# Performance work log

Measured on AMD Instinct MI355X. Metric: run time of the kernel, lower is better.

## Reference

```python
import jax, jax.numpy as jnp
import numpy as np

T, K, H, I, E = 8192, 2, 1024, 2816, 8


def setup_inputs() -> dict:
    key = jax.random.key(0)
    k1, k2, k3, k4, k5 = jax.random.split(key, 5)
    hidden_states = jax.random.normal(k1, (T, H), dtype=jnp.float32)
    expert_routing_table = jax.random.randint(k2, (T, K), 0, E)
    router_weights = jax.random.uniform(k3, (T, K), dtype=jnp.float32)
    # permuted_weights=True: weights stored so forward is x @ w
    # w13: fused gate+up proj [E, H, 2I]; w2: down proj [E, I, H]
    w13 = jax.random.normal(k4, (E, H, 2 * I), dtype=jnp.float32) * (1.0 / np.sqrt(H))
    w2 = jax.random.normal(k5, (E, I, H), dtype=jnp.float32) * (1.0 / np.sqrt(I))
    return {
        "hidden_states": hidden_states,
        "expert_routing_table": expert_routing_table,
        "router_weights": router_weights,
        "w13": w13,
        "w2": w2,
    }


def reference(hidden_states, expert_routing_table, router_weights, w13, w2):
    # Semantics of hpu.mixture_of_experts with activation='silu':
    # out[t] = sum_k rw[t,k] * ( (silu(x@w1g[e]) * (x@w1u[e])) @ w2[e] ), e = table[t,k]
    n_experts = w13.shape[0]
    inter = w2.shape[1]
    # per-token combine coefficient for each expert: [T, E]
    onehot = jax.nn.one_hot(expert_routing_table, n_experts, dtype=hidden_states.dtype)  # [T,K,E]
    coeff = jnp.einsum("tke,tk->te", onehot, router_weights)
    out = jnp.zeros_like(hidden_states)
    for e in range(n_experts):
        gu = hidden_states @ w13[e]            # [T, 2I]
        gate, up = gu[:, :inter], gu[:, inter:]
        h = jax.nn.silu(gate) * up             # [T, I]
        out = out + coeff[:, e:e + 1] * (h @ w2[e])
    return out
```

## Files before the change

### kernel.cpp

```cpp
#include <hip/hip_runtime.h>

typedef unsigned short u16;
typedef unsigned int u32;
typedef __bf16 bf16x8 __attribute__((ext_vector_type(8)));
typedef float f32x4 __attribute__((ext_vector_type(4)));
typedef u16 u16x4 __attribute__((ext_vector_type(4)));
typedef u16 u16x8 __attribute__((ext_vector_type(8)));

#define T_TOK 8192
#define HDIM 1024
#define IDIM 2816
#define NEXP 8
#define NPAIR (T_TOK * 2)
#define MAXRB 71

#define XB_OFF   (147456u)
#define W13T_OFF (XB_OFF + 16777216u)
#define W2T_OFF  (W13T_OFF + 92274688u)
#define H_OFF    (W2T_OFF + 46137344u)
#define WS_NEED  ((size_t)H_OFF + 102367232u)

__device__ __forceinline__ u16 f2bf(float f) {
  u32 u = __builtin_bit_cast(u32, f);
  u32 r = u + 0x7fffu + ((u >> 16) & 1u);
  return (u16)(r >> 16);
}

#define GLD16(g, l) __builtin_amdgcn_global_load_lds( \
    (const __attribute__((address_space(1))) void*)(g), \
    (__attribute__((address_space(3))) void*)(l), 16, 0, 0)

#define WAITVM(N) asm volatile("s_waitcnt vmcnt(" #N ")" ::: "memory")

__device__ __forceinline__ void pbar() {
  __builtin_amdgcn_sched_barrier(0);
  asm volatile("" ::: "memory");
  __builtin_amdgcn_s_barrier();
  asm volatile("" ::: "memory");
  __builtin_amdgcn_sched_barrier(0);
}

__global__ void init_meta(int* meta) {
  if (threadIdx.x < 16) meta[threadIdx.x] = 0;
}

__global__ void count_k(const int* __restrict__ routing, int* __restrict__ meta) {
  int i = blockIdx.x * 256 + threadIdx.x;
  if (i < NPAIR) atomicAdd(&meta[routing[i]], 1);
}

__global__ void scan_k(int* __restrict__ meta) {
  if (threadIdx.x == 0) {
    int rb = 0;
    for (int e = 0; e < NEXP; ++e) {
      meta[16 + e] = rb * 256;
      int nrb = (meta[e] + 255) >> 8;
      for (int i = 0; i < nrb; ++i) meta[32 + rb + i] = e;
      rb += nrb;
    }
    meta[24] = rb;
  }
}

__global__ void fill_pairs(int* __restrict__ pairs) {
  pairs[blockIdx.x * 256 + threadIdx.x] = -1;
}

__global__ void scatter_k(const int* __restrict__ routing, int* __restrict__ meta,
                          int* __restrict__ pairs, int* __restrict__ inv) {
  int i = blockIdx.x * 256 + threadIdx.x;
  if (i < NPAIR) {
    int e = routing[i];
    int pos = atomicAdd(&meta[8 + e], 1);
    int row = meta[16 + e] + pos;
    pairs[row] = i;
    inv[i] = row;
  }
}

__global__ void conv_x(const float* __restrict__ in, u16* __restrict__ out) {
  int i = blockIdx.x * 256 + threadIdx.x;
  float4 a = ((const float4*)in)[2 * i];
  float4 b = ((const float4*)in)[2 * i + 1];
  u16x8 o = { f2bf(a.x), f2bf(a.y), f2bf(a.z), f2bf(a.w),
              f2bf(b.x), f2bf(b.y), f2bf(b.z), f2bf(b.w) };
  ((u16x8*)out)[i] = o;
}

__global__ void transpose_cvt(const float* __restrict__ in, u16* __restrict__ out,
                              int R, int C) {
  __shared__ float tile[64][68];
  size_t base = (size_t)blockIdx.z * (size_t)R * (size_t)C;
  in += base; out += base;
  int t = threadIdx.x;
  int r0 = blockIdx.y * 64, c0 = blockIdx.x * 64;
  int lr = t >> 4, lc4 = (t & 15) * 4;
#pragma unroll
  for (int p = 0; p < 4; ++p) {
    float4 v = *(const float4*)&in[(size_t)(r0 + p * 16 + lr) * C + c0 + lc4];
    tile[p * 16 + lr][lc4] = v.x; tile[p * 16 + lr][lc4 + 1] = v.y;
    tile[p * 16 + lr][lc4 + 2] = v.z; tile[p * 16 + lr][lc4 + 3] = v.w;
  }
  __syncthreads();
  int oc = t >> 2, g0 = (t & 3) * 2;
#pragma unroll
  for (int gg = 0; gg < 2; ++gg) {
    int g = g0 + gg;
    u16x8 o = { f2bf(tile[g * 8 + 0][oc]), f2bf(tile[g * 8 + 1][oc]),
                f2bf(tile[g * 8 + 2][oc]), f2bf(tile[g * 8 + 3][oc]),
                f2bf(tile[g * 8 + 4][oc]), f2bf(tile[g * 8 + 5][oc]),
                f2bf(tile[g * 8 + 6][oc]), f2bf(tile[g * 8 + 7][oc]) };
    *(u16x8*)&out[(size_t)(c0 + oc) * R + r0 + g * 8] = o;
  }
}

__global__ __launch_bounds__(512, 2) void gemm1_k(
    const u16* __restrict__ Xb, const u16* __restrict__ W13T,
    const int* __restrict__ pairs, const int* __restrict__ meta,
    const float* __restrict__ rwf, u16* __restrict__ Hb) {
  int lin = blockIdx.x + 22 * blockIdx.y;
  int xcd = lin & 7, slot = lin >> 3;
  int flat = (xcd < 2) ? xcd * 196 + slot : 392 + (xcd - 2) * 195 + slot;
  int bx = flat / 71, rb = flat % 71;
  if (rb >= meta[24]) return;
  const int e = meta[32 + rb];
  const int bn0 = bx * 128;
  const int tid = threadIdx.x, lane = tid & 63, w = tid >> 6;
  const int wr = w >> 1, wc = w & 1;
  const int rowBase = rb * 256;

  __shared__ __align__(16) u16 lds[65536];
  char* const lb = (char*)lds;

  const int sr = tid >> 3;
  const int swk = ((tid & 7) << 4) ^ ((sr & 7) << 4);
  const u16* aS[4];
#pragma unroll
  for (int h = 0; h < 2; ++h)
#pragma unroll
    for (int j = 0; j < 2; ++j) {
      int pr = pairs[rowBase + h * 128 + j * 64 + sr];
      int tok = pr < 0 ? 0 : (pr >> 1);
      aS[h * 2 + j] = Xb + (size_t)tok * HDIM + (swk >> 1);
    }
  const u16* wBase = W13T + (size_t)e * (2 * IDIM) * HDIM;
  const u16* gS[2]; const u16* uS[2];
#pragma unroll
  for (int j = 0; j < 2; ++j) {
    int r = j * 64 + sr;
    gS[j] = wBase + (size_t)(bn0 + r) * HDIM + (swk >> 1);
    uS[j] = wBase + (size_t)(IDIM + bn0 + r) * HDIM + (swk >> 1);
  }

#define STG_A(b, h, kt) { GLD16(aS[(h)*2+0] + (kt)*64, lb + (b)*32768 + (h)*16384 + tid*16); \
                          GLD16(aS[(h)*2+1] + (kt)*64, lb + (b)*32768 + (h)*16384 + 8192 + tid*16); }
#define STG_G(b, kt)    { GLD16(gS[0] + (kt)*64, lb + 65536 + (b)*16384 + tid*16); \
                          GLD16(gS[1] + (kt)*64, lb + 65536 + (b)*16384 + 8192 + tid*16); }
#define STG_U(b, kt)    { GLD16(uS[0] + (kt)*64, lb + 98304 + (b)*16384 + tid*16); \
                          GLD16(uS[1] + (kt)*64, lb + 98304 + (b)*16384 + 8192 + tid*16); }

  const int l15 = lane & 15, l4 = lane >> 4, l7 = lane & 7;
  const int ko0 = (l4 * 16) ^ (l7 << 4);
  const int ko1 = (64 + l4 * 16) ^ (l7 << 4);
  const int aFB = (wr >> 1) * 16384 + ((wr & 1) * 64 + l15) * 128;
  const int bFB = (wc * 64 + l15) * 128;

#define LDAF(d, b, mf, ko) d = *(const bf16x8*)(lb + (b)*32768 + aFB + (mf)*2048 + (ko))
#define LDGF(d, b, nf, ko) d = *(const bf16x8*)(lb + 65536 + (b)*16384 + bFB + (nf)*2048 + (ko))
#define LDUF(d, b, nf, ko) d = *(const bf16x8*)(lb + 98304 + (b)*16384 + bFB + (nf)*2048 + (ko))

#define MF16(ACC, A, B) \
  _Pragma("unroll") for (int mf = 0; mf < 4; ++mf) \
  _Pragma("unroll") for (int nf = 0; nf < 4; ++nf) \
    ACC[mf][nf] = __builtin_amdgcn_mfma_f32_16x16x32_bf16(A[mf], B[nf], ACC[mf][nf], 0, 0, 0);

  f32x4 accG[4][4], accU[4][4];
  const f32x4 fz = {0.f, 0.f, 0.f, 0.f};
#pragma unroll
  for (int i = 0; i < 4; ++i)
#pragma unroll
    for (int j = 0; j < 4; ++j) { accG[i][j] = fz; accU[i][j] = fz; }

  STG_A(0, 0, 0); STG_A(0, 1, 0); STG_G(0, 0); STG_U(0, 0); STG_A(1, 0, 1);
  WAITVM(4);
  pbar();

  bf16x8 a0[4], a1[4], g0[4], g1[4], u0[4], u1[4];
  for (int i = 0; i < 8; ++i) {
    const int t1 = 2 * i + 1;
    const int n2 = (2 * i + 2) & 15, n3 = (2 * i + 3) & 15;
#pragma unroll
    for (int f = 0; f < 4; ++f) { LDAF(a0[f], 0, f, ko0); LDGF(g0[f], 0, f, ko0); }
    STG_A(1, 1, t1);
    pbar();
    __builtin_amdgcn_s_setprio(1); MF16(accG, a0, g0); __builtin_amdgcn_s_setprio(0);
    WAITVM(4);
    pbar();
#pragma unroll
    for (int f = 0; f < 4; ++f) { LDUF(u0[f], 0, f, ko0); LDAF(a1[f], 0, f, ko1); }
    STG_G(1, t1);
    pbar();
    __builtin_amdgcn_s_setprio(1); MF16(accU, a0, u0); __builtin_amdgcn_s_setprio(0);
    pbar();
#pragma unroll
    for (int f = 0; f < 4; ++f) { LDGF(g1[f], 0, f, ko1); LDUF(u1[f], 0, f, ko1); }
    STG_U(1, t1);
    pbar();
    __builtin_amdgcn_s_setprio(1); MF16(accG, a1, g1); __builtin_amdgcn_s_setprio(0);
    pbar();
    STG_A(0, 0, n2);
    pbar();
    __builtin_amdgcn_s_setprio(1); MF16(accU, a1, u1); __builtin_amdgcn_s_setprio(0);
    WAITVM(4);
    pbar();
#pragma unroll
    for (int f = 0; f < 4; ++f) { LDAF(a0[f], 1, f, ko0); LDGF(g0[f], 1, f, ko0); }
    STG_A(0, 1, n2);
    pbar();
    __builtin_amdgcn_s_setprio(1); MF16(accG, a0, g0); __builtin_amdgcn_s_setprio(0);
    WAITVM(4);
    pbar();
#pragma unroll
    for (int f = 0; f < 4; ++f) { LDUF(u0[f], 1, f, ko0); LDAF(a1[f], 1, f, ko1); }
    STG_G(0, n2);
    pbar();
    __builtin_amdgcn_s_setprio(1); MF16(accU, a0, u0); __builtin_amdgcn_s_setprio(0);
    pbar();
#pragma unroll
    for (int f = 0; f < 4; ++f) { LDGF(g1[f], 1, f, ko1); LDUF(u1[f], 1, f, ko1); }
    STG_U(0, n2);
    pbar();
    __builtin_amdgcn_s_setprio(1); MF16(accG, a1, g1); __builtin_amdgcn_s_setprio(0);
    pbar();
    STG_A(1, 0, n3);
    pbar();
    __builtin_amdgcn_s_setprio(1); MF16(accU, a1, u1); __builtin_amdgcn_s_setprio(0);
    WAITVM(4);
    pbar();
  }
#undef STG_A
#undef STG_G
#undef STG_U
#undef LDAF
#undef LDGF
#undef LDUF

  const int ct = l4;
#pragma unroll
  for (int mf = 0; mf < 4; ++mf) {
#pragma unroll
    for (int j = 0; j < 4; ++j) {
      int m = wr * 64 + mf * 16 + ct * 4 + j;
      int pr = rowBase + m;
      int pair = pairs[pr];
      float rw = pair >= 0 ? rwf[pair] : 0.f;
      u16* hrow = Hb + (size_t)pr * IDIM + bn0 + wc * 64 + l15;
#pragma unroll
      for (int nf = 0; nf < 4; ++nf) {
        float g = accG[mf][nf][j], u = accU[mf][nf][j];
        float s = g / (1.f + __expf(-g));
        hrow[nf * 16] = f2bf(s * u * rw);
      }
    }
  }
}

__global__ __launch_bounds__(256, 2) void gemm2_k(
    const u16* __restrict__ Hb, const u16* __restrict__ W2T,
    const int* __restrict__ meta, float* __restrict__ part) {
  int lin = blockIdx.y + 142 * blockIdx.x;
  int xcd = lin & 7, slot = lin >> 3;
  int flat = xcd * 142 + slot;
  int bx = flat / 142, rb2 = flat % 142;
  if (rb2 >= meta[24] * 2) return;
  const int e = meta[32 + (rb2 >> 1)];
  const int bn0 = bx * 128;
  const int tid = threadIdx.x, lane = tid & 63, w = tid >> 6;
  const int wr = w >> 1, wc = w & 1;
  const int rowBase = rb2 * 128;

  __shared__ __align__(16) u16 lds2[32768];
  char* const lb = (char*)lds2;

  const int sr = tid >> 3;
  const int swk = ((tid & 7) << 4) ^ ((sr & 7) << 4);
  const u16* aS[4]; const u16* bS[4];
#pragma unroll
  for (int j = 0; j < 4; ++j) {
    aS[j] = Hb + (size_t)(rowBase + j * 32 + sr) * IDIM + (swk >> 1);
    bS[j] = W2T + (size_t)e * HDIM * IDIM + (size_t)(bn0 + j * 32 + sr) * IDIM + (swk >> 1);
  }

#define STG_A2(b, kt) { GLD16(aS[0] + (kt)*64, lb + (b)*16384 + tid*16); \
                        GLD16(aS[1] + (kt)*64, lb + (b)*16384 + 4096 + tid*16); \
                        GLD16(aS[2] + (kt)*64, lb + (b)*16384 + 8192 + tid*16); \
                        GLD16(aS[3] + (kt)*64, lb + (b)*16384 + 12288 + tid*16); }
#define STG_B2(b, kt) { GLD16(bS[0] + (kt)*64, lb + 32768 + (b)*16384 + tid*16); \
                        GLD16(bS[1] + (kt)*64, lb + 32768 + (b)*16384 + 4096 + tid*16); \
                        GLD16(bS[2] + (kt)*64, lb + 32768 + (b)*16384 + 8192 + tid*16); \
                        GLD16(bS[3] + (kt)*64, lb + 32768 + (b)*16384 + 12288 + tid*16); }

  const int l15 = lane & 15, l4 = lane >> 4, l7 = lane & 7;
  const int ko0 = (l4 * 16) ^ (l7 << 4);
  const int ko1 = (64 + l4 * 16) ^ (l7 << 4);
  const int aFB = (wr * 64 + l15) * 128;
  const int bFB = (wc * 64 + l15) * 128;

#define LDAF2(d, b, mf, ko) d = *(const bf16x8*)(lb + (b)*16384 + aFB + (mf)*2048 + (ko))
#define LDBF2(d, b, nf, ko) d = *(const bf16x8*)(lb + 32768 + (b)*16384 + bFB + (nf)*2048 + (ko))

#define MF16v(A, B) \
  _Pragma("unroll") for (int mf = 0; mf < 4; ++mf) \
  _Pragma("unroll") for (int nf = 0; nf < 4; ++nf) \
    acc[mf][nf] = __builtin_amdgcn_mfma_f32_16x16x32_bf16(A[mf], B[nf], acc[mf][nf], 0, 0, 0);

  f32x4 acc[4][4];
  const f32x4 fz = {0.f, 0.f, 0.f, 0.f};
#pragma unroll
  for (int i = 0; i < 4; ++i)
#pragma unroll
    for (int j = 0; j < 4; ++j) acc[i][j] = fz;

  STG_A2(0, 0); STG_B2(0, 0); STG_A2(1, 1);
  WAITVM(4);
  pbar();

  bf16x8 a0[4], a1[4], b0[4], b1[4];
  for (int i = 0; i < 22; ++i) {
    const int t1 = 2 * i + 1;
    const int nt0 = (2 * i + 2 < 44) ? 2 * i + 2 : 0;
    const int nt1 = (2 * i + 3 < 44) ? 2 * i + 3 : 0;
#pragma unroll
    for (int f = 0; f < 4; ++f) { LDAF2(a0[f], 0, f, ko0); LDAF2(a1[f], 0, f, ko1);
                                  LDBF2(b0[f], 0, f, ko0); LDBF2(b1[f], 0, f, ko1); }
    STG_B2(1, t1);
    pbar();
    __builtin_amdgcn_s_setprio(1); MF16v(a0, b0); __builtin_amdgcn_s_setprio(0);
    pbar();
    STG_A2(0, nt0);
    pbar();
    __builtin_amdgcn_s_setprio(1); MF16v(a1, b1); __builtin_amdgcn_s_setprio(0);
    WAITVM(4);
    pbar();
#pragma unroll
    for (int f = 0; f < 4; ++f) { LDAF2(a0[f], 1, f, ko0); LDAF2(a1[f], 1, f, ko1);
                                  LDBF2(b0[f], 1, f, ko0); LDBF2(b1[f], 1, f, ko1); }
    STG_B2(0, nt0);
    pbar();
    __builtin_amdgcn_s_setprio(1); MF16v(a0, b0); __builtin_amdgcn_s_setprio(0);
    pbar();
    STG_A2(1, nt1);
    pbar();
    __builtin_amdgcn_s_setprio(1); MF16v(a1, b1); __builtin_amdgcn_s_setprio(0);
    WAITVM(4);
    pbar();
  }
#undef STG_A2
#undef STG_B2
#undef LDAF2
#undef LDBF2

  WAITVM(0);
  const int ct = l4;
#pragma unroll
  for (int mf = 0; mf < 4; ++mf) {
#pragma unroll
    for (int j = 0; j < 4; ++j) {
      int m = rowBase + wr * 64 + mf * 16 + ct * 4 + j;
      float* prow = part + (size_t)m * HDIM + bn0 + wc * 64 + l15;
#pragma unroll
      for (int nf = 0; nf < 4; ++nf) prow[nf * 16] = acc[mf][nf][j];
    }
  }
}

__global__ void reduce_k(const float* __restrict__ part, const int* __restrict__ inv,
                         float* __restrict__ out) {
  int t = blockIdx.x;
  int c = threadIdx.x * 4;
  int r0 = inv[2 * t], r1 = inv[2 * t + 1];
  float4 a = *(const float4*)&part[(size_t)r0 * HDIM + c];
  float4 b = *(const float4*)&part[(size_t)r1 * HDIM + c];
  float4 o = { a.x + b.x, a.y + b.y, a.z + b.z, a.w + b.w };
  *(float4*)&out[(size_t)t * HDIM + c] = o;
}

extern "C" void kernel_launch(void* const* d_in, const int* in_sizes, int n_in,
                              void* d_out, int out_size, void* d_ws, size_t ws_size,
                              hipStream_t stream) {
  const float* X = (const float*)d_in[0];
  const int* routing = (const int*)d_in[1];
  const float* rwf = (const float*)d_in[2];
  const float* w13 = (const float*)d_in[3];
  const float* w2 = (const float*)d_in[4];
  float* out = (float*)d_out;
  char* ws = (char*)d_ws;

  if (ws_size < WS_NEED) {
    hipMemsetAsync(d_out, 0, (size_t)T_TOK * HDIM * sizeof(float), stream);
    return;
  }

  int* meta = (int*)ws;
  int* pairs = (int*)(ws + 1024);
  int* inv = (int*)(ws + 73728);
  u16* Xb = (u16*)(ws + XB_OFF);
  u16* W13T = (u16*)(ws + W13T_OFF);
  u16* W2T = (u16*)(ws + W2T_OFF);
  u16* Hb = (u16*)(ws + H_OFF);
  float* part = (float*)(ws + W13T_OFF);

  init_meta<<<1, 64, 0, stream>>>(meta);
  count_k<<<NPAIR / 256, 256, 0, stream>>>(routing, meta);
  scan_k<<<1, 64, 0, stream>>>(meta);
  fill_pairs<<<MAXRB, 256, 0, stream>>>(pairs);
  scatter_k<<<NPAIR / 256, 256, 0, stream>>>(routing, meta, pairs, inv);
  conv_x<<<(T_TOK * HDIM / 8) / 256, 256, 0, stream>>>(X, Xb);
  transpose_cvt<<<dim3(5632 / 64, 1024 / 64, NEXP), 256, 0, stream>>>(w13, W13T, 1024, 5632);
  transpose_cvt<<<dim3(1024 / 64, 2816 / 64, NEXP), 256, 0, stream>>>(w2, W2T, 2816, 1024);
  gemm1_k<<<dim3(22, MAXRB), 512, 0, stream>>>(Xb, W13T, pairs, meta, rwf, Hb);
  gemm2_k<<<dim3(8, 2 * MAXRB), 256, 0, stream>>>(Hb, W2T, meta, part);
  reduce_k<<<T_TOK, 256, 0, stream>>>(part, inv, out);
}
```

Before: 574.2 us.

## Restructure gemm1 warp tiling to 2x4 with interleaved gate/up B tile; swizzle transpose LDS

The gate/up GEMM kernel changes its wave layout from 4x2 to 2x4 waves. Each wave now covers 128 rows by 64 interleaved gate/up columns, and gate and up rows are loaded into a single combined B tile. This cuts LDS fragment loads per MFMA (A fragments reused across the gate and up columns) and simplifies the staging schedule into a two-stage macro. Separately, the transpose-convert kernel XOR-swizzles its shared-memory tile columns to reduce bank conflicts on the column reads. The new pipeline changes the wait/barrier ordering and could expose load latency differently.

```diff
diff --git a/kernel.cpp b/kernel.cpp
--- a/kernel.cpp
+++ b/kernel.cpp
@@ -87,6 +87,7 @@
   ((u16x8*)out)[i] = o;
 }
 
+#define TSW(r, c) (((((c) >> 2) ^ ((((r) >> 4) & 3) << 2)) << 2) | ((c) & 3))
 __global__ void transpose_cvt(const float* __restrict__ in, u16* __restrict__ out,
                               int R, int C) {
   __shared__ float tile[64][68];
@@ -94,22 +95,24 @@
   in += base; out += base;
   int t = threadIdx.x;
   int r0 = blockIdx.y * 64, c0 = blockIdx.x * 64;
-  int lr = t >> 4, lc4 = (t & 15) * 4;
+  int lr = t >> 4, cb = t & 15;
 #pragma unroll
   for (int p = 0; p < 4; ++p) {
-    float4 v = *(const float4*)&in[(size_t)(r0 + p * 16 + lr) * C + c0 + lc4];
-    tile[p * 16 + lr][lc4] = v.x; tile[p * 16 + lr][lc4 + 1] = v.y;
-    tile[p * 16 + lr][lc4 + 2] = v.z; tile[p * 16 + lr][lc4 + 3] = v.w;
+    int row = p * 16 + lr;
+    float4 v = *(const float4*)&in[(size_t)(r0 + row) * C + c0 + cb * 4];
+    int pc = ((cb ^ ((p & 3) << 2)) << 2);
+    tile[row][pc] = v.x; tile[row][pc + 1] = v.y;
+    tile[row][pc + 2] = v.z; tile[row][pc + 3] = v.w;
   }
   __syncthreads();
   int oc = t >> 2, g0 = (t & 3) * 2;
 #pragma unroll
   for (int gg = 0; gg < 2; ++gg) {
     int g = g0 + gg;
-    u16x8 o = { f2bf(tile[g * 8 + 0][oc]), f2bf(tile[g * 8 + 1][oc]),
-                f2bf(tile[g * 8 + 2][oc]), f2bf(tile[g * 8 + 3][oc]),
-                f2bf(tile[g * 8 + 4][oc]), f2bf(tile[g * 8 + 5][oc]),
-                f2bf(tile[g * 8 + 6][oc]), f2bf(tile[g * 8 + 7][oc]) };
+    u16x8 o = { f2bf(tile[g * 8 + 0][TSW(g * 8 + 0, oc)]), f2bf(tile[g * 8 + 1][TSW(g * 8 + 1, oc)]),
+                f2bf(tile[g * 8 + 2][TSW(g * 8 + 2, oc)]), f2bf(tile[g * 8 + 3][TSW(g * 8 + 3, oc)]),
+                f2bf(tile[g * 8 + 4][TSW(g * 8 + 4, oc)]), f2bf(tile[g * 8 + 5][TSW(g * 8 + 5, oc)]),
+                f2bf(tile[g * 8 + 6][TSW(g * 8 + 6, oc)]), f2bf(tile[g * 8 + 7][TSW(g * 8 + 7, oc)]) };
     *(u16x8*)&out[(size_t)(c0 + oc) * R + r0 + g * 8] = o;
   }
 }
@@ -126,140 +129,110 @@
   const int e = meta[32 + rb];
   const int bn0 = bx * 128;
   const int tid = threadIdx.x, lane = tid & 63, w = tid >> 6;
-  const int wr = w >> 1, wc = w & 1;
+  const int wr = w >> 2, wc = w & 3;
   const int rowBase = rb * 256;
 
   __shared__ __align__(16) u16 lds[65536];
   char* const lb = (char*)lds;
 
-  const int sr = tid >> 3;
-  const int swk = ((tid & 7) << 4) ^ ((sr & 7) << 4);
-  const u16* aS[4];
-#pragma unroll
-  for (int h = 0; h < 2; ++h)
-#pragma unroll
-    for (int j = 0; j < 2; ++j) {
-      int pr = pairs[rowBase + h * 128 + j * 64 + sr];
-      int tok = pr < 0 ? 0 : (pr >> 1);
-      aS[h * 2 + j] = Xb + (size_t)tok * HDIM + (swk >> 1);
-    }
+  const int tr = tid >> 3;
+  const int swk = ((tid & 7) << 4) ^ ((tr & 7) << 4);
+  const u16* aS[4]; const u16* bS[4];
   const u16* wBase = W13T + (size_t)e * (2 * IDIM) * HDIM;
-  const u16* gS[2]; const u16* uS[2];
-#pragma unroll
-  for (int j = 0; j < 2; ++j) {
-    int r = j * 64 + sr;
-    gS[j] = wBase + (size_t)(bn0 + r) * HDIM + (swk >> 1);
-    uS[j] = wBase + (size_t)(IDIM + bn0 + r) * HDIM + (swk >> 1);
-  }
-
-#define STG_A(b, h, kt) { GLD16(aS[(h)*2+0] + (kt)*64, lb + (b)*32768 + (h)*16384 + tid*16); \
-                          GLD16(aS[(h)*2+1] + (kt)*64, lb + (b)*32768 + (h)*16384 + 8192 + tid*16); }
-#define STG_G(b, kt)    { GLD16(gS[0] + (kt)*64, lb + 65536 + (b)*16384 + tid*16); \
-                          GLD16(gS[1] + (kt)*64, lb + 65536 + (b)*16384 + 8192 + tid*16); }
-#define STG_U(b, kt)    { GLD16(uS[0] + (kt)*64, lb + 98304 + (b)*16384 + tid*16); \
-                          GLD16(uS[1] + (kt)*64, lb + 98304 + (b)*16384 + 8192 + tid*16); }
+#pragma unroll
+  for (int s = 0; s < 4; ++s) {
+    int pr = pairs[rowBase + s * 64 + tr];
+    int tok = pr < 0 ? 0 : (pr >> 1);
+    aS[s] = Xb + (size_t)tok * HDIM + (swk >> 1);
+    bS[s] = wBase + (size_t)((tr >> 5) * IDIM + bn0 + s * 32 + (tr & 31)) * HDIM + (swk >> 1);
+  }
+
+#define STGA(b, h, kt) { GLD16(aS[(h)*2]   + (kt)*64, lb + (b)*32768 + (h)*16384 + tid*16); \
+                         GLD16(aS[(h)*2+1] + (kt)*64, lb + (b)*32768 + (h)*16384 + 8192 + tid*16); }
+#define STGB(b, h, kt) { GLD16(bS[(h)*2]   + (kt)*64, lb + 65536 + (b)*32768 + (h)*16384 + tid*16); \
+                         GLD16(bS[(h)*2+1] + (kt)*64, lb + 65536 + (b)*32768 + (h)*16384 + 8192 + tid*16); }
 
   const int l15 = lane & 15, l4 = lane >> 4, l7 = lane & 7;
   const int ko0 = (l4 * 16) ^ (l7 << 4);
   const int ko1 = (64 + l4 * 16) ^ (l7 << 4);
-  const int aFB = (wr >> 1) * 16384 + ((wr & 1) * 64 + l15) * 128;
-  const int bFB = (wc * 64 + l15) * 128;
-
-#define LDAF(d, b, mf, ko) d = *(const bf16x8*)(lb + (b)*32768 + aFB + (mf)*2048 + (ko))
-#define LDGF(d, b, nf, ko) d = *(const bf16x8*)(lb + 65536 + (b)*16384 + bFB + (nf)*2048 + (ko))
-#define LDUF(d, b, nf, ko) d = *(const bf16x8*)(lb + 98304 + (b)*16384 + bFB + (nf)*2048 + (ko))
-
-#define MF16(ACC, A, B) \
+  const int aFB = wr * 16384 + l15 * 128;
+  const int bFB = 65536 + (wc * 64 + l15) * 128;
+
+#define LDA(d, b, mh, mf, ko) d = *(const bf16x8*)(lb + (b)*32768 + aFB + (mh)*8192 + (mf)*2048 + (ko))
+#define LDB(d, b, nf, ko)     d = *(const bf16x8*)(lb + (b)*32768 + bFB + (nf)*2048 + (ko))
+
+#define MFQ(mh, A, B) \
   _Pragma("unroll") for (int mf = 0; mf < 4; ++mf) \
   _Pragma("unroll") for (int nf = 0; nf < 4; ++nf) \
-    ACC[mf][nf] = __builtin_amdgcn_mfma_f32_16x16x32_bf16(A[mf], B[nf], ACC[mf][nf], 0, 0, 0);
-
-  f32x4 accG[4][4], accU[4][4];
+    acc[(mh)*4+mf][nf] = __builtin_amdgcn_mfma_f32_16x16x32_bf16(A[mf], B[nf], acc[(mh)*4+mf][nf], 0, 0, 0);
+
+  f32x4 acc[8][4];
   const f32x4 fz = {0.f, 0.f, 0.f, 0.f};
 #pragma unroll
-  for (int i = 0; i < 4; ++i)
-#pragma unroll
-    for (int j = 0; j < 4; ++j) { accG[i][j] = fz; accU[i][j] = fz; }
-
-  STG_A(0, 0, 0); STG_A(0, 1, 0); STG_G(0, 0); STG_U(0, 0); STG_A(1, 0, 1);
+  for (int i = 0; i < 8; ++i)
+#pragma unroll
+    for (int j = 0; j < 4; ++j) acc[i][j] = fz;
+
+  STGB(0, 0, 0); STGB(0, 1, 0); STGA(0, 0, 0); STGA(0, 1, 0); STGB(1, 0, 1); STGB(1, 1, 1);
   WAITVM(4);
   pbar();
 
-  bf16x8 a0[4], a1[4], g0[4], g1[4], u0[4], u1[4];
-  for (int i = 0; i < 8; ++i) {
-    const int t1 = 2 * i + 1;
-    const int n2 = (2 * i + 2) & 15, n3 = (2 * i + 3) & 15;
-#pragma unroll
-    for (int f = 0; f < 4; ++f) { LDAF(a0[f], 0, f, ko0); LDGF(g0[f], 0, f, ko0); }
-    STG_A(1, 1, t1);
-    pbar();
-    __builtin_amdgcn_s_setprio(1); MF16(accG, a0, g0); __builtin_amdgcn_s_setprio(0);
-    WAITVM(4);
-    pbar();
-#pragma unroll
-    for (int f = 0; f < 4; ++f) { LDUF(u0[f], 0, f, ko0); LDAF(a1[f], 0, f, ko1); }
-    STG_G(1, t1);
-    pbar();
-    __builtin_amdgcn_s_setprio(1); MF16(accU, a0, u0); __builtin_amdgcn_s_setprio(0);
-    pbar();
-#pragma unroll
-    for (int f = 0; f < 4; ++f) { LDGF(g1[f], 0, f, ko1); LDUF(u1[f], 0, f, ko1); }
-    STG_U(1, t1);
-    pbar();
-    __builtin_amdgcn_s_setprio(1); MF16(accG, a1, g1); __builtin_amdgcn_s_setprio(0);
-    pbar();
-    STG_A(0, 0, n2);
-    pbar();
-    __builtin_amdgcn_s_setprio(1); MF16(accU, a1, u1); __builtin_amdgcn_s_setprio(0);
-    WAITVM(4);
-    pbar();
-#pragma unroll
-    for (int f = 0; f < 4; ++f) { LDAF(a0[f], 1, f, ko0); LDGF(g0[f], 1, f, ko0); }
-    STG_A(0, 1, n2);
-    pbar();
-    __builtin_amdgcn_s_setprio(1); MF16(accG, a0, g0); __builtin_amdgcn_s_setprio(0);
-    WAITVM(4);
-    pbar();
-#pragma unroll
-    for (int f = 0; f < 4; ++f) { LDUF(u0[f], 1, f, ko0); LDAF(a1[f], 1, f, ko1); }
-    STG_G(0, n2);
-    pbar();
-    __builtin_amdgcn_s_setprio(1); MF16(accU, a0, u0); __builtin_amdgcn_s_setprio(0);
-    pbar();
-#pragma unroll
-    for (int f = 0; f < 4; ++f) { LDGF(g1[f], 1, f, ko1); LDUF(u1[f], 1, f, ko1); }
-    STG_U(0, n2);
-    pbar();
-    __builtin_amdgcn_s_setprio(1); MF16(accG, a1, g1); __builtin_amdgcn_s_setprio(0);
-    pbar();
-    STG_A(1, 0, n3);
-    pbar();
-    __builtin_amdgcn_s_setprio(1); MF16(accU, a1, u1); __builtin_amdgcn_s_setprio(0);
-    WAITVM(4);
-    pbar();
-  }
-#undef STG_A
-#undef STG_G
-#undef STG_U
-#undef LDAF
-#undef LDGF
-#undef LDUF
+  bf16x8 aF[4], b0F[4], b1F[4];
+#define ITER1(b, t1, t2) { \
+     \
+    _Pragma("unroll") for (int f = 0; f < 4; ++f) { LDA(aF[f], b, 0, f, ko0); LDB(b0F[f], b, f, ko0); } \
+    STGA((b)^1, 0, t1); \
+    pbar(); \
+    __builtin_amdgcn_s_setprio(1); MFQ(0, aF, b0F); __builtin_amdgcn_s_setprio(0); \
+    pbar(); \
+     \
+    _Pragma("unroll") for (int f = 0; f < 4; ++f) { LDA(aF[f], b, 0, f, ko1); LDB(b1F[f], b, f, ko1); } \
+    STGA((b)^1, 1, t1); \
+    pbar(); \
+    __builtin_amdgcn_s_setprio(1); MFQ(0, aF, b1F); __builtin_amdgcn_s_setprio(0); \
+    pbar(); \
+     \
+    _Pragma("unroll") for (int f = 0; f < 4; ++f) { LDA(aF[f], b, 1, f, ko0); } \
+    STGB(b, 0, t2); \
+    pbar(); \
+    __builtin_amdgcn_s_setprio(1); MFQ(1, aF, b0F); __builtin_amdgcn_s_setprio(0); \
+    pbar(); \
+     \
+    _Pragma("unroll") for (int f = 0; f < 4; ++f) { LDA(aF[f], b, 1, f, ko1); } \
+    STGB(b, 1, t2); \
+    pbar(); \
+    __builtin_amdgcn_s_setprio(1); MFQ(1, aF, b1F); __builtin_amdgcn_s_setprio(0); \
+    WAITVM(4); \
+    pbar(); \
+  }
+
+  for (int jj = 0; jj < 8; ++jj) {
+    const int ta = (2 * jj + 1) & 15, tb = (2 * jj + 2) & 15, tc = (2 * jj + 3) & 15;
+    ITER1(0, ta, tb);
+    ITER1(1, tb, tc);
+  }
+#undef ITER1
+#undef STGA
+#undef STGB
+#undef LDA
+#undef LDB
+#undef MFQ
 
   const int ct = l4;
 #pragma unroll
-  for (int mf = 0; mf < 4; ++mf) {
+  for (int mf = 0; mf < 8; ++mf) {
 #pragma unroll
     for (int j = 0; j < 4; ++j) {
-      int m = wr * 64 + mf * 16 + ct * 4 + j;
+      int m = wr * 128 + mf * 16 + ct * 4 + j;
       int pr = rowBase + m;
       int pair = pairs[pr];
       float rw = pair >= 0 ? rwf[pair] : 0.f;
-      u16* hrow = Hb + (size_t)pr * IDIM + bn0 + wc * 64 + l15;
-#pragma unroll
-      for (int nf = 0; nf < 4; ++nf) {
-        float g = accG[mf][nf][j], u = accU[mf][nf][j];
-        float s = g / (1.f + __expf(-g));
-        hrow[nf * 16] = f2bf(s * u * rw);
+      u16* hrow = Hb + (size_t)pr * IDIM + bn0 + wc * 32 + l15;
+#pragma unroll
+      for (int g = 0; g < 2; ++g) {
+        float gv = acc[mf][g][j], uv = acc[mf][g + 2][j];
+        float s = gv / (1.f + __expf(-gv));
+        hrow[g * 16] = f2bf(s * uv * rw);
       }
     }
   }
@@ -359,6 +332,7 @@
 #undef STG_B2
 #undef LDAF2
 #undef LDBF2
+#undef MF16v
 
   WAITVM(0);
   const int ct = l4;
```

New measurement: 579.8 us. No clear change (+1.0%).
